# Optimization experiments

Hardware: AMD Instinct MI355X
Metric: run time of the kernel (lower is better)

The kernel has to match this reference:

```python
import jax, jax.numpy as jnp
import numpy as np

D_MODEL = 1024
NHEAD = 16
HEAD_DIM = D_MODEL // NHEAD
B, L = 4, 4096
LN_EPS = 1e-5


def setup_inputs() -> dict:
    key = jax.random.key(0)
    ks = jax.random.split(key, 8)
    x = jax.random.normal(ks[0], (B, L, D_MODEL), dtype=jnp.float32)
    sin = jnp.zeros((L, HEAD_DIM), dtype=jnp.float32)
    cos = jnp.zeros((L, HEAD_DIM), dtype=jnp.float32)
    # decay[:,1,0] is read as per-head lambda in (0,1)
    decay = jax.random.uniform(ks[1], (NHEAD, 2, 1), dtype=jnp.float32)
    scale = 0.02
    Wq = jax.random.normal(ks[2], (D_MODEL, D_MODEL), dtype=jnp.float32) * scale
    Wv = jax.random.normal(ks[3], (D_MODEL, D_MODEL), dtype=jnp.float32) * scale
    Wo = jax.random.normal(ks[4], (D_MODEL, D_MODEL), dtype=jnp.float32) * scale
    Wg = jax.random.normal(ks[5], (D_MODEL, D_MODEL), dtype=jnp.float32) * scale
    ln_g = jnp.ones((D_MODEL,), dtype=jnp.float32)
    ln_b = jnp.zeros((D_MODEL,), dtype=jnp.float32)
    return {"x": x, "sin": sin, "cos": cos, "decay": decay,
            "Wq": Wq, "Wv": Wv, "Wo": Wo, "Wg": Wg,
            "ln_g": ln_g, "ln_b": ln_b}


def _retention(v, lam):
    # v: [B,L,H,Dh], lam: [H] -> cumulative decayed sum over L
    def step(state, v_t):  # state,[B,H,Dh]
        state = lam[None, :, None] * state + v_t
        return state, state
    v_l_first = jnp.swapaxes(v, 0, 1)  # [L,B,H,Dh]
    init = jnp.zeros(v_l_first.shape[1:], dtype=v.dtype)
    _, states = jax.lax.scan(step, init, v_l_first)
    return jnp.swapaxes(states, 0, 1)  # [B,L,H,Dh]


def reference(x, sin, cos, decay, Wq, Wv, Wo, Wg, ln_g, ln_b):
    del sin, cos  # discarded by the module
    Bx, Lx, D = x.shape
    H = decay.shape[0]
    Dh = D // H
    q = (x @ Wq.T).reshape(Bx, Lx, H, Dh)
    v = (x @ Wv.T).reshape(Bx, Lx, H, Dh)
    lam = decay[:, 1, 0]  # [H]
    state = _retention(v, lam)  # [B,L,H,Dh]
    y = (q * state).reshape(Bx, Lx, D)
    # LayerNorm over last dim
    mu = jnp.mean(y, axis=-1, keepdims=True)
    var = jnp.mean(jnp.square(y - mu), axis=-1, keepdims=True)
    y = (y - mu) * jax.lax.rsqrt(var + LN_EPS) * ln_g + ln_b
    gate = jax.nn.silu(x @ Wg.T)
    y = y * gate
    return y @ Wo.T
```

## Files before the change

### kernel.cpp

```cpp
#include <hip/hip_runtime.h>

#define DM    1024
#define LSEQ  4096
#define BATCH 4
#define MROWS (BATCH * LSEQ)
#define MD    ((size_t)MROWS * DM)
#define DD    ((size_t)DM * DM)
#define CHUNK 32
#define NCH   (LSEQ / CHUNK)
#define NCHAIN (BATCH * DM)

typedef __attribute__((ext_vector_type(4))) float  f32x4;
typedef __attribute__((ext_vector_type(8))) __bf16 bf16x8;
typedef __attribute__((ext_vector_type(4))) __bf16 bf16x4;

__device__ __forceinline__ void gload_lds16(const void* g, void* l) {
  __builtin_amdgcn_global_load_lds(
      (const __attribute__((address_space(1))) void*)g,
      (__attribute__((address_space(3))) void*)l, 16, 0, 0);
}

__global__ __launch_bounds__(256) void cvt_bf16(const float* __restrict__ in,
                                                __bf16* __restrict__ out) {
  size_t i = ((size_t)blockIdx.x * 256 + threadIdx.x) * 4;
  f32x4 f = *(const f32x4*)(in + i);
  bf16x4 o;
#pragma unroll
  for (int j = 0; j < 4; ++j) o[j] = (__bf16)f[j];
  *(bf16x4*)(out + i) = o;
}

__global__ __launch_bounds__(256) void cvt_w(const float* __restrict__ s0,
                                             const float* __restrict__ s1,
                                             const float* __restrict__ s2,
                                             const float* __restrict__ s3,
                                             __bf16* __restrict__ dst) {
  const float* sp = (blockIdx.z == 0) ? s0 : (blockIdx.z == 1) ? s1
                  : (blockIdx.z == 2) ? s2 : s3;
  size_t i = ((size_t)blockIdx.x * 256 + threadIdx.x) * 4;
  f32x4 f = *(const f32x4*)(sp + i);
  bf16x4 o;
#pragma unroll
  for (int j = 0; j < 4; ++j) o[j] = (__bf16)f[j];
  *(bf16x4*)(dst + (size_t)blockIdx.z * DD + i) = o;
}


__device__ __forceinline__ int swz(int b) { return b ^ ((b >> 3) & 0x70); }

__device__ __forceinline__ bf16x8 ldf(const char* tile, int row, int k) {
  int lin = (row << 7) + (k << 1);
  return *(const bf16x8*)(tile + swz(lin));
}

__device__ __forceinline__ void stageA_half(const __bf16* Abase, char* tileA,
                                            int h, int k0, int t) {
#pragma unroll
  for (int is = 0; is < 2; ++is) {
    int d = h * 16384 + is * 8192 + t * 16;
    int l = swz(d);
    int lds_r = l >> 7, cb = l & 127;
    int g = ((lds_r >> 6) & 1) * 128 + h * 64 + (lds_r & 63);
    gload_lds16((const char*)Abase + (size_t)g * (DM * 2) + k0 * 2 + cb, tileA + d);
  }
}
__device__ __forceinline__ void stageB_half(const __bf16* Bbase, char* tileB,
                                            int h, int k0, int t) {
#pragma unroll
  for (int is = 0; is < 2; ++is) {
    int d = h * 16384 + is * 8192 + t * 16;
    int l = swz(d);
    int lds_r = l >> 7, cb = l & 127;
    int g = ((lds_r >> 5) & 3) * 64 + h * 32 + (lds_r & 31);
    gload_lds16((const char*)Bbase + (size_t)g * (DM * 2) + k0 * 2 + cb, tileB + d);
  }
}

template <typename OutT>
__global__ __launch_bounds__(512, 2) void gemm_nt(const __bf16* __restrict__ A,
                                                  const __bf16* __restrict__ Wb,
                                                  OutT* __restrict__ Cb) {
  constexpr int K = DM, N = DM, NT = K / 64;
  __shared__ __attribute__((aligned(128))) char lds[131072];

  const __bf16* Wp = Wb + (size_t)blockIdx.z * DD;
  OutT* Cp = Cb + (size_t)blockIdx.z * MD;

  const int orig = blockIdx.y * 4 + blockIdx.x;
  const int sid = (orig & 7) * 32 + (orig >> 3);
  const int bx = sid & 3, by = sid >> 2;
  const int m0 = by * 256, n0 = bx * 256;

  const int t = threadIdx.x, lane = t & 63, wv = t >> 6;
  const int wr = wv >> 2, wc = wv & 3;
  const int lrow = lane & 15, lk8 = (lane >> 4) * 8;

  const __bf16* Abase = A + (size_t)m0 * K;
  const __bf16* Bbase = Wp + (size_t)n0 * K;

  f32x4 acc[8][4] = {};
  bf16x8 a[4][2];
  bf16x8 bq[2][2][2];

  char* buf0 = lds;
  char* buf1 = lds + 65536;

  stageA_half(Abase, buf0,         0, 0, t);
  stageB_half(Bbase, buf0 + 32768, 0, 0, t);
  stageB_half(Bbase, buf0 + 32768, 1, 0, t);
  stageA_half(Abase, buf0,         1, 0, t);
  stageA_half(Abase, buf1,         0, 64, t);
  stageB_half(Bbase, buf1 + 32768, 0, 64, t);
  stageB_half(Bbase, buf1 + 32768, 1, 64, t);
  stageA_half(Abase, buf1,         1, 64, t);
  asm volatile("s_waitcnt vmcnt(12)\n\ts_barrier" ::: "memory");

#define LDA_(mh)                                                        \
  _Pragma("unroll") for (int mf = 0; mf < 4; ++mf)                      \
  _Pragma("unroll") for (int ks = 0; ks < 2; ++ks)                      \
    a[mf][ks] = ldf(At, (mh) * 128 + wr * 64 + mf * 16 + lrow, ks * 32 + lk8);
#define LDB_(nh)                                                        \
  _Pragma("unroll") for (int nf = 0; nf < 2; ++nf)                      \
  _Pragma("unroll") for (int ks = 0; ks < 2; ++ks)                      \
    bq[nh][nf][ks] = ldf(Bt, (nh) * 128 + wc * 32 + nf * 16 + lrow, ks * 32 + lk8);
#define MFMA16_(mh, nh)                                                 \
  __builtin_amdgcn_s_setprio(1);                                        \
  _Pragma("unroll") for (int mf = 0; mf < 4; ++mf)                      \
  _Pragma("unroll") for (int nf = 0; nf < 2; ++nf)                      \
  _Pragma("unroll") for (int ks = 0; ks < 2; ++ks)                      \
    acc[(mh) * 4 + mf][(nh) * 2 + nf] = __builtin_amdgcn_mfma_f32_16x16x32_bf16( \
        a[mf][ks], bq[nh][nf][ks], acc[(mh) * 4 + mf][(nh) * 2 + nf], 0, 0, 0); \
  __builtin_amdgcn_s_setprio(0);
#define VMBAR_(n)                                                       \
  asm volatile("s_waitcnt vmcnt(" #n ")\n\ts_barrier" ::: "memory");
#define BAR_                                                            \
  asm volatile("s_barrier" ::: "memory");

#pragma unroll 1
  for (int kt = 0; kt < NT; ++kt) {
    char* bufc = lds + (kt & 1) * 65536;
    const char* At = bufc;
    const char* Bt = bufc + 32768;
    const int k2 = (kt + 2) << 6;
    const bool s2 = (kt + 2 < NT);

    LDA_(0); LDB_(0);
    MFMA16_(0, 0);
    if (kt < NT - 1) { VMBAR_(10); } else { VMBAR_(2); }

    if (s2) {
      stageA_half(Abase, bufc,         0, k2, t);
      stageB_half(Bbase, bufc + 32768, 0, k2, t);
    }
    LDB_(1);
    MFMA16_(0, 1);
    if (s2) { VMBAR_(12); } else if (kt == NT - 2) { VMBAR_(8); } else { VMBAR_(0); }

    if (s2) stageB_half(Bbase, bufc + 32768, 1, k2, t);
    LDA_(1);
    MFMA16_(1, 0);
    BAR_;

    if (s2) stageA_half(Abase, bufc, 1, k2, t);
    MFMA16_(1, 1);
    if (s2) { VMBAR_(12); } else if (kt == NT - 2) { VMBAR_(4); } else { VMBAR_(0); }
  }
#undef LDA_
#undef LDB_
#undef MFMA16_
#undef VMBAR_
#undef BAR_

#pragma unroll
  for (int mi = 0; mi < 8; ++mi) {
    int r0 = m0 + wr * 128 + (mi >> 2) * 64 + (mi & 3) * 16 + (lane >> 4) * 4;
#pragma unroll
    for (int ni = 0; ni < 4; ++ni) {
      int c0 = n0 + wc * 64 + (ni >> 1) * 32 + (ni & 1) * 16 + (lane & 15);
#pragma unroll
      for (int j = 0; j < 4; ++j) {
        float v = acc[mi][ni][j];
        if constexpr (__is_same(OutT, float))
          Cp[(size_t)(r0 + j) * N + c0] = v;
        else
          Cp[(size_t)(r0 + j) * N + c0] = (__bf16)v;
      }
    }
  }
}

__global__ __launch_bounds__(256) void scan_sum(const __bf16* __restrict__ v,
                                                float* __restrict__ csum,
                                                const float* __restrict__ decay) {
  int tid = blockIdx.x * 256 + threadIdx.x;
  int dg = tid & 255;
  int b  = (tid >> 8) & 3;
  int c  = tid >> 10;
  int d0 = dg * 4;
  float lam = decay[((d0 >> 6) << 1) + 1];
  f32x4 s = {0.f, 0.f, 0.f, 0.f};
  size_t base = ((size_t)b * LSEQ + (size_t)c * CHUNK) * DM + d0;
  for (int t = 0; t < CHUNK; ++t) {
    bf16x4 vv = *(const bf16x4*)(v + base);
    f32x4 vf = {(float)vv[0], (float)vv[1], (float)vv[2], (float)vv[3]};
    s = lam * s + vf;
    base += DM;
  }
  *(f32x4*)(csum + (size_t)c * NCHAIN + b * DM + d0) = s;
}

__global__ __launch_bounds__(256) void scan2(const float* __restrict__ csum,
                                             float* __restrict__ carry,
                                             const float* __restrict__ decay) {
  int i = blockIdx.x * 256 + threadIdx.x;
  int ch0 = i * 4;
  int d0 = ch0 & (DM - 1);
  float lam = decay[((d0 >> 6) << 1) + 1];
  float l2 = lam * lam, l4 = l2 * l2, l8 = l4 * l4, l16 = l8 * l8;
  float lamC = l16 * l16;
  f32x4 cs = {0.f, 0.f, 0.f, 0.f};
  for (int c = 0; c < NCH; ++c) {
    *(f32x4*)(carry + (size_t)c * NCHAIN + ch0) = cs;
    f32x4 sm = *(const f32x4*)(csum + (size_t)c * NCHAIN + ch0);
    cs = lamC * cs + sm;
  }
}

__global__ __launch_bounds__(256) void fuse_chunk(
    const __bf16* __restrict__ qb, const __bf16* __restrict__ vb,
    const __bf16* __restrict__ gb, const float* __restrict__ carry,
    const float* __restrict__ decay, const float* __restrict__ ln_g,
    const float* __restrict__ ln_b, __bf16* __restrict__ y2) {
  const int blk = blockIdx.x;
  const int b = blk >> 7, c = blk & 127;
  const int t = threadIdx.x, lane = t & 63, wv = t >> 6;
  const int d0 = t * 4;
  const float lam = decay[((d0 >> 6) << 1) + 1];
  f32x4 s = *(const f32x4*)(carry + (size_t)c * NCHAIN + b * DM + d0);
  const size_t base0 = ((size_t)b * LSEQ + (size_t)c * CHUNK) * DM + d0;

  __shared__ float sbs[2][32][4];
  __shared__ float stats[32][2];

  f32x4 y[32];
#pragma unroll
  for (int r = 0; r < 32; ++r) {
    size_t base = base0 + (size_t)r * DM;
    bf16x4 v4 = *(const bf16x4*)(vb + base);
    bf16x4 q4 = *(const bf16x4*)(qb + base);
    f32x4 vf = {(float)v4[0], (float)v4[1], (float)v4[2], (float)v4[3]};
    s = lam * s + vf;
    f32x4 yy;
    float su = 0.f, sq = 0.f;
#pragma unroll
    for (int i = 0; i < 4; ++i) {
      float val = (float)q4[i] * s[i];
      yy[i] = val; su += val; sq += val * val;
    }
    y[r] = yy;
#pragma unroll
    for (int o = 32; o > 0; o >>= 1) {
      su += __shfl_xor(su, o);
      sq += __shfl_xor(sq, o);
    }
    if (lane == 0) { sbs[0][r][wv] = su; sbs[1][r][wv] = sq; }
  }
  __syncthreads();
  if (t < 32) {
    float su = sbs[0][t][0] + sbs[0][t][1] + sbs[0][t][2] + sbs[0][t][3];
    float sq = sbs[1][t][0] + sbs[1][t][1] + sbs[1][t][2] + sbs[1][t][3];
    float mu = su * (1.0f / DM);
    float var = sq * (1.0f / DM) - mu * mu;
    stats[t][0] = mu;
    stats[t][1] = rsqrtf(fmaxf(var, 0.0f) + 1e-5f);
  }
  __syncthreads();

  f32x4 lg = *(const f32x4*)(ln_g + d0);
  f32x4 lb = *(const f32x4*)(ln_b + d0);
#pragma unroll
  for (int r = 0; r < 32; ++r) {
    size_t base = base0 + (size_t)r * DM;
    bf16x4 g4 = *(const bf16x4*)(gb + base);
    const float mu = stats[r][0], rstd = stats[r][1];
    bf16x4 o4;
#pragma unroll
    for (int i = 0; i < 4; ++i) {
      float gv = (float)g4[i];
      float gate = gv / (1.0f + __expf(-gv));
      o4[i] = (__bf16)(fmaf((y[r][i] - mu) * rstd, lg[i], lb[i]) * gate);
    }
    *(bf16x4*)(y2 + base) = o4;
  }
}

extern "C" void kernel_launch(void* const* d_in, const int* in_sizes, int n_in,
                              void* d_out, int out_size, void* d_ws, size_t ws_size,
                              hipStream_t stream) {
  const float* x     = (const float*)d_in[0];
  const float* decay = (const float*)d_in[3];
  const float* Wq    = (const float*)d_in[4];
  const float* Wv    = (const float*)d_in[5];
  const float* Wo    = (const float*)d_in[6];
  const float* Wg    = (const float*)d_in[7];
  const float* lng   = (const float*)d_in[8];
  const float* lnb   = (const float*)d_in[9];
  float* out = (float*)d_out;

  char* ws = (char*)d_ws;
  size_t off = 0;
  auto alloc = [&](size_t bytes) -> void* {
    void* p = ws + off;
    off += (bytes + 255) & ~(size_t)255;
    return p;
  };
  __bf16* xb   = (__bf16*)alloc(MD * 2);
  __bf16* w4   = (__bf16*)alloc(4 * DD * 2);
  __bf16* qvg  = (__bf16*)alloc(3 * MD * 2);
  __bf16* y2b  = (__bf16*)alloc(MD * 2);
  float*  csum = (float*)alloc((size_t)NCH * NCHAIN * 4);
  float*  cry  = (float*)alloc((size_t)NCH * NCHAIN * 4);

  cvt_bf16<<<(int)(MD / 1024), 256, 0, stream>>>(x, xb);
  cvt_w<<<dim3((unsigned)(DD / 1024), 1, 4), 256, 0, stream>>>(Wq, Wv, Wg, Wo, w4);

  gemm_nt<__bf16><<<dim3(4, MROWS / 256, 3), 512, 0, stream>>>(xb, w4, qvg);

  scan_sum<<<(BATCH * NCH * (DM / 4)) / 256, 256, 0, stream>>>(qvg + MD, csum, decay);
  scan2<<<(NCHAIN / 4) / 256, 256, 0, stream>>>(csum, cry, decay);

  fuse_chunk<<<BATCH * NCH, 256, 0, stream>>>(qvg, qvg + MD, qvg + 2 * MD, cry,
                                              decay, lng, lnb, y2b);

  gemm_nt<float><<<dim3(4, MROWS / 256, 1), 512, 0, stream>>>(y2b, w4 + 3 * DD, out);
}
```

Measured before the change: 215.4 us.

## Replace tuned 256x256 swizzled GEMM with simple 128x128 double-buffered GEMM

Replaces the hand-scheduled 256x256-tile, 512-thread GEMM with a simpler 128x128-tile, 256-thread kernel. It uses K-step 32, unswizzled LDS tiles and a plain double buffer with a full vmcnt/lgkmcnt wait and barrier each iteration. The aim is higher occupancy (4 blocks per CU) and simpler code. In exchange it loses the LDS swizzle, so bank conflicts become likely, and it gets less data reuse per tile, more barriers, and weaker overlap of loads with MFMA work.

```diff
diff --git a/kernel.cpp b/kernel.cpp
--- a/kernel.cpp
+++ b/kernel.cpp
@@ -46,140 +46,79 @@
 }
 
 
-__device__ __forceinline__ int swz(int b) { return b ^ ((b >> 3) & 0x70); }
-
-__device__ __forceinline__ bf16x8 ldf(const char* tile, int row, int k) {
-  int lin = (row << 7) + (k << 1);
-  return *(const bf16x8*)(tile + swz(lin));
-}
-
-__device__ __forceinline__ void stageA_half(const __bf16* Abase, char* tileA,
-                                            int h, int k0, int t) {
+__device__ __forceinline__ void stage_tile(const __bf16* __restrict__ base,
+                                           __bf16* lds, int k0, int t) {
 #pragma unroll
   for (int is = 0; is < 2; ++is) {
-    int d = h * 16384 + is * 8192 + t * 16;
-    int l = swz(d);
-    int lds_r = l >> 7, cb = l & 127;
-    int g = ((lds_r >> 6) & 1) * 128 + h * 64 + (lds_r & 63);
-    gload_lds16((const char*)Abase + (size_t)g * (DM * 2) + k0 * 2 + cb, tileA + d);
-  }
-}
-__device__ __forceinline__ void stageB_half(const __bf16* Bbase, char* tileB,
-                                            int h, int k0, int t) {
-#pragma unroll
-  for (int is = 0; is < 2; ++is) {
-    int d = h * 16384 + is * 8192 + t * 16;
-    int l = swz(d);
-    int lds_r = l >> 7, cb = l & 127;
-    int g = ((lds_r >> 5) & 3) * 64 + h * 32 + (lds_r & 31);
-    gload_lds16((const char*)Bbase + (size_t)g * (DM * 2) + k0 * 2 + cb, tileB + d);
+    int e = is * 2048 + t * 8;
+    int r = e >> 5, c = e & 31;
+    gload_lds16(base + (size_t)r * DM + k0 + c, lds + e);
   }
 }
 
 template <typename OutT>
-__global__ __launch_bounds__(512, 2) void gemm_nt(const __bf16* __restrict__ A,
+__global__ __launch_bounds__(256, 4) void gemm_nt(const __bf16* __restrict__ A,
                                                   const __bf16* __restrict__ Wb,
                                                   OutT* __restrict__ Cb) {
-  constexpr int K = DM, N = DM, NT = K / 64;
-  __shared__ __attribute__((aligned(128))) char lds[131072];
+  constexpr int K = DM, N = DM, NT = K / 32;
+  __shared__ __bf16 As[2][128 * 32];
+  __shared__ __bf16 Bs[2][128 * 32];
 
   const __bf16* Wp = Wb + (size_t)blockIdx.z * DD;
   OutT* Cp = Cb + (size_t)blockIdx.z * MD;
 
-  const int orig = blockIdx.y * 4 + blockIdx.x;
-  const int sid = (orig & 7) * 32 + (orig >> 3);
-  const int bx = sid & 3, by = sid >> 2;
-  const int m0 = by * 256, n0 = bx * 256;
+  const int orig = blockIdx.y * 8 + blockIdx.x;
+  const int sid = (orig & 7) * 128 + (orig >> 3);
+  const int bx = sid & 7, by = sid >> 3;
+  const int m0 = by * 128, n0 = bx * 128;
 
   const int t = threadIdx.x, lane = t & 63, wv = t >> 6;
-  const int wr = wv >> 2, wc = wv & 3;
-  const int lrow = lane & 15, lk8 = (lane >> 4) * 8;
+  const int wr = wv >> 1, wc = wv & 1;
+  const int lrow = lane & 15, koff = (lane >> 4) * 8;
 
   const __bf16* Abase = A + (size_t)m0 * K;
   const __bf16* Bbase = Wp + (size_t)n0 * K;
 
-  f32x4 acc[8][4] = {};
-  bf16x8 a[4][2];
-  bf16x8 bq[2][2][2];
-
-  char* buf0 = lds;
-  char* buf1 = lds + 65536;
-
-  stageA_half(Abase, buf0,         0, 0, t);
-  stageB_half(Bbase, buf0 + 32768, 0, 0, t);
-  stageB_half(Bbase, buf0 + 32768, 1, 0, t);
-  stageA_half(Abase, buf0,         1, 0, t);
-  stageA_half(Abase, buf1,         0, 64, t);
-  stageB_half(Bbase, buf1 + 32768, 0, 64, t);
-  stageB_half(Bbase, buf1 + 32768, 1, 64, t);
-  stageA_half(Abase, buf1,         1, 64, t);
-  asm volatile("s_waitcnt vmcnt(12)\n\ts_barrier" ::: "memory");
-
-#define LDA_(mh)                                                        \
-  _Pragma("unroll") for (int mf = 0; mf < 4; ++mf)                      \
-  _Pragma("unroll") for (int ks = 0; ks < 2; ++ks)                      \
-    a[mf][ks] = ldf(At, (mh) * 128 + wr * 64 + mf * 16 + lrow, ks * 32 + lk8);
-#define LDB_(nh)                                                        \
-  _Pragma("unroll") for (int nf = 0; nf < 2; ++nf)                      \
-  _Pragma("unroll") for (int ks = 0; ks < 2; ++ks)                      \
-    bq[nh][nf][ks] = ldf(Bt, (nh) * 128 + wc * 32 + nf * 16 + lrow, ks * 32 + lk8);
-#define MFMA16_(mh, nh)                                                 \
-  __builtin_amdgcn_s_setprio(1);                                        \
-  _Pragma("unroll") for (int mf = 0; mf < 4; ++mf)                      \
-  _Pragma("unroll") for (int nf = 0; nf < 2; ++nf)                      \
-  _Pragma("unroll") for (int ks = 0; ks < 2; ++ks)                      \
-    acc[(mh) * 4 + mf][(nh) * 2 + nf] = __builtin_amdgcn_mfma_f32_16x16x32_bf16( \
-        a[mf][ks], bq[nh][nf][ks], acc[(mh) * 4 + mf][(nh) * 2 + nf], 0, 0, 0); \
-  __builtin_amdgcn_s_setprio(0);
-#define VMBAR_(n)                                                       \
-  asm volatile("s_waitcnt vmcnt(" #n ")\n\ts_barrier" ::: "memory");
-#define BAR_                                                            \
-  asm volatile("s_barrier" ::: "memory");
+  f32x4 acc[4][4] = {};
+  bf16x8 a[4], b[4];
+
+  stage_tile(Abase, As[0], 0, t);
+  stage_tile(Bbase, Bs[0], 0, t);
+  asm volatile("s_waitcnt vmcnt(0)\n\ts_barrier" ::: "memory");
 
 #pragma unroll 1
   for (int kt = 0; kt < NT; ++kt) {
-    char* bufc = lds + (kt & 1) * 65536;
-    const char* At = bufc;
-    const char* Bt = bufc + 32768;
-    const int k2 = (kt + 2) << 6;
-    const bool s2 = (kt + 2 < NT);
-
-    LDA_(0); LDB_(0);
-    MFMA16_(0, 0);
-    if (kt < NT - 1) { VMBAR_(10); } else { VMBAR_(2); }
-
-    if (s2) {
-      stageA_half(Abase, bufc,         0, k2, t);
-      stageB_half(Bbase, bufc + 32768, 0, k2, t);
-    }
-    LDB_(1);
-    MFMA16_(0, 1);
-    if (s2) { VMBAR_(12); } else if (kt == NT - 2) { VMBAR_(8); } else { VMBAR_(0); }
-
-    if (s2) stageB_half(Bbase, bufc + 32768, 1, k2, t);
-    LDA_(1);
-    MFMA16_(1, 0);
-    BAR_;
-
-    if (s2) stageA_half(Abase, bufc, 1, k2, t);
-    MFMA16_(1, 1);
-    if (s2) { VMBAR_(12); } else if (kt == NT - 2) { VMBAR_(4); } else { VMBAR_(0); }
-  }
-#undef LDA_
-#undef LDB_
-#undef MFMA16_
-#undef VMBAR_
-#undef BAR_
-
-#pragma unroll
-  for (int mi = 0; mi < 8; ++mi) {
-    int r0 = m0 + wr * 128 + (mi >> 2) * 64 + (mi & 3) * 16 + (lane >> 4) * 4;
-#pragma unroll
-    for (int ni = 0; ni < 4; ++ni) {
-      int c0 = n0 + wc * 64 + (ni >> 1) * 32 + (ni & 1) * 16 + (lane & 15);
+    const int cur = kt & 1, nxt = cur ^ 1;
+    if (kt + 1 < NT) {
+      stage_tile(Abase, As[nxt], (kt + 1) * 32, t);
+      stage_tile(Bbase, Bs[nxt], (kt + 1) * 32, t);
+    }
+#pragma unroll
+    for (int mf = 0; mf < 4; ++mf)
+      a[mf] = *(const bf16x8*)&As[cur][(wr * 64 + mf * 16 + lrow) * 32 + koff];
+#pragma unroll
+    for (int nf = 0; nf < 4; ++nf)
+      b[nf] = *(const bf16x8*)&Bs[cur][(wc * 64 + nf * 16 + lrow) * 32 + koff];
+    __builtin_amdgcn_s_setprio(1);
+#pragma unroll
+    for (int mf = 0; mf < 4; ++mf)
+#pragma unroll
+      for (int nf = 0; nf < 4; ++nf)
+        acc[mf][nf] = __builtin_amdgcn_mfma_f32_16x16x32_bf16(
+            a[mf], b[nf], acc[mf][nf], 0, 0, 0);
+    __builtin_amdgcn_s_setprio(0);
+    asm volatile("s_waitcnt vmcnt(0) lgkmcnt(0)\n\ts_barrier" ::: "memory");
+  }
+
+#pragma unroll
+  for (int mf = 0; mf < 4; ++mf) {
+    int r0 = m0 + wr * 64 + mf * 16 + (lane >> 4) * 4;
+#pragma unroll
+    for (int nf = 0; nf < 4; ++nf) {
+      int c0 = n0 + wc * 64 + nf * 16 + (lane & 15);
 #pragma unroll
       for (int j = 0; j < 4; ++j) {
-        float v = acc[mi][ni][j];
+        float v = acc[mf][nf][j];
         if constexpr (__is_same(OutT, float))
           Cp[(size_t)(r0 + j) * N + c0] = v;
         else
@@ -324,7 +263,7 @@
   cvt_bf16<<<(int)(MD / 1024), 256, 0, stream>>>(x, xb);
   cvt_w<<<dim3((unsigned)(DD / 1024), 1, 4), 256, 0, stream>>>(Wq, Wv, Wg, Wo, w4);
 
-  gemm_nt<__bf16><<<dim3(4, MROWS / 256, 3), 512, 0, stream>>>(xb, w4, qvg);
+  gemm_nt<__bf16><<<dim3(8, MROWS / 128, 3), 256, 0, stream>>>(xb, w4, qvg);
 
   scan_sum<<<(BATCH * NCH * (DM / 4)) / 256, 256, 0, stream>>>(qvg + MD, csum, decay);
   scan2<<<(NCHAIN / 4) / 256, 256, 0, stream>>>(csum, cry, decay);
@@ -332,5 +271,5 @@
   fuse_chunk<<<BATCH * NCH, 256, 0, stream>>>(qvg, qvg + MD, qvg + 2 * MD, cry,
                                               decay, lng, lnb, y2b);
 
-  gemm_nt<float><<<dim3(4, MROWS / 256, 1), 512, 0, stream>>>(y2b, w4 + 3 * DD, out);
-}
+  gemm_nt<float><<<dim3(8, MROWS / 128, 1), 256, 0, stream>>>(y2b, w4 + 3 * DD, out);
+}
```

Result: slower. 237.4 us (+10.2%).

## Restructure GEMM main loop with single-tile LDS prefetch and register double-buffering

Applied to the files above, without the earlier changes.

Replaces the half-tile, two-steps-ahead LDS staging with whole-tile staging one step ahead. It adds ping-pong register fragments, so LDS reads for the next half overlap the MFMAs of the current half. Explicit lgkmcnt waits and sched_barriers pin the instruction order, and launch bounds drop to one block per CU to relax register limits. The aim is to hide LDS-read latency behind matrix math. The cost is a full vmcnt(0) barrier every iteration and a shorter global-load lookahead.

```diff
diff --git a/kernel.cpp b/kernel.cpp
--- a/kernel.cpp
+++ b/kernel.cpp
@@ -53,31 +53,19 @@
   return *(const bf16x8*)(tile + swz(lin));
 }
 
-__device__ __forceinline__ void stageA_half(const __bf16* Abase, char* tileA,
-                                            int h, int k0, int t) {
-#pragma unroll
-  for (int is = 0; is < 2; ++is) {
-    int d = h * 16384 + is * 8192 + t * 16;
+__device__ __forceinline__ void stage_tile(const __bf16* __restrict__ base,
+                                           char* tile, int k0, int t) {
+#pragma unroll
+  for (int is = 0; is < 4; ++is) {
+    int d = is * 8192 + t * 16;
     int l = swz(d);
-    int lds_r = l >> 7, cb = l & 127;
-    int g = ((lds_r >> 6) & 1) * 128 + h * 64 + (lds_r & 63);
-    gload_lds16((const char*)Abase + (size_t)g * (DM * 2) + k0 * 2 + cb, tileA + d);
-  }
-}
-__device__ __forceinline__ void stageB_half(const __bf16* Bbase, char* tileB,
-                                            int h, int k0, int t) {
-#pragma unroll
-  for (int is = 0; is < 2; ++is) {
-    int d = h * 16384 + is * 8192 + t * 16;
-    int l = swz(d);
-    int lds_r = l >> 7, cb = l & 127;
-    int g = ((lds_r >> 5) & 3) * 64 + h * 32 + (lds_r & 31);
-    gload_lds16((const char*)Bbase + (size_t)g * (DM * 2) + k0 * 2 + cb, tileB + d);
+    int row = l >> 7, cb = l & 127;
+    gload_lds16((const char*)base + (size_t)row * (DM * 2) + k0 * 2 + cb, tile + d);
   }
 }
 
 template <typename OutT>
-__global__ __launch_bounds__(512, 2) void gemm_nt(const __bf16* __restrict__ A,
+__global__ __launch_bounds__(512, 1) void gemm_nt(const __bf16* __restrict__ A,
                                                   const __bf16* __restrict__ Wb,
                                                   OutT* __restrict__ Cb) {
   constexpr int K = DM, N = DM, NT = K / 64;
@@ -99,77 +87,68 @@
   const __bf16* Bbase = Wp + (size_t)n0 * K;
 
   f32x4 acc[8][4] = {};
-  bf16x8 a[4][2];
-  bf16x8 bq[2][2][2];
-
-  char* buf0 = lds;
-  char* buf1 = lds + 65536;
-
-  stageA_half(Abase, buf0,         0, 0, t);
-  stageB_half(Bbase, buf0 + 32768, 0, 0, t);
-  stageB_half(Bbase, buf0 + 32768, 1, 0, t);
-  stageA_half(Abase, buf0,         1, 0, t);
-  stageA_half(Abase, buf1,         0, 64, t);
-  stageB_half(Bbase, buf1 + 32768, 0, 64, t);
-  stageB_half(Bbase, buf1 + 32768, 1, 64, t);
-  stageA_half(Abase, buf1,         1, 64, t);
-  asm volatile("s_waitcnt vmcnt(12)\n\ts_barrier" ::: "memory");
-
-#define LDA_(mh)                                                        \
+  bf16x8 a0[4][2], a1[4][2];
+  bf16x8 b0[2][2], b1[2][2];
+
+#define LDA_(dst, mh, tile)                                             \
   _Pragma("unroll") for (int mf = 0; mf < 4; ++mf)                      \
   _Pragma("unroll") for (int ks = 0; ks < 2; ++ks)                      \
-    a[mf][ks] = ldf(At, (mh) * 128 + wr * 64 + mf * 16 + lrow, ks * 32 + lk8);
-#define LDB_(nh)                                                        \
+    dst[mf][ks] = ldf(tile, wr * 128 + (mh) * 64 + mf * 16 + lrow, ks * 32 + lk8);
+#define LDB_(dst, nh, tile)                                             \
   _Pragma("unroll") for (int nf = 0; nf < 2; ++nf)                      \
   _Pragma("unroll") for (int ks = 0; ks < 2; ++ks)                      \
-    bq[nh][nf][ks] = ldf(Bt, (nh) * 128 + wc * 32 + nf * 16 + lrow, ks * 32 + lk8);
-#define MFMA16_(mh, nh)                                                 \
+    dst[nf][ks] = ldf(tile, wc * 64 + (nh) * 32 + nf * 16 + lrow, ks * 32 + lk8);
+#define MFMA16_(av, bv, mh, nh)                                         \
   __builtin_amdgcn_s_setprio(1);                                        \
   _Pragma("unroll") for (int mf = 0; mf < 4; ++mf)                      \
   _Pragma("unroll") for (int nf = 0; nf < 2; ++nf)                      \
   _Pragma("unroll") for (int ks = 0; ks < 2; ++ks)                      \
     acc[(mh) * 4 + mf][(nh) * 2 + nf] = __builtin_amdgcn_mfma_f32_16x16x32_bf16( \
-        a[mf][ks], bq[nh][nf][ks], acc[(mh) * 4 + mf][(nh) * 2 + nf], 0, 0, 0); \
+        av[mf][ks], bv[nf][ks], acc[(mh) * 4 + mf][(nh) * 2 + nf], 0, 0, 0); \
   __builtin_amdgcn_s_setprio(0);
-#define VMBAR_(n)                                                       \
-  asm volatile("s_waitcnt vmcnt(" #n ")\n\ts_barrier" ::: "memory");
-#define BAR_                                                            \
-  asm volatile("s_barrier" ::: "memory");
+#define SB_ __builtin_amdgcn_sched_barrier(0);
+#define LGKM_(n)                                                        \
+  asm volatile("s_waitcnt lgkmcnt(" #n ")" ::: "memory"); SB_
+
+  stage_tile(Abase, lds,         0, t);
+  stage_tile(Bbase, lds + 32768, 0, t);
+  asm volatile("s_waitcnt vmcnt(0)\n\ts_barrier" ::: "memory");
+  SB_
+  LDB_(b0, 0, lds + 32768); SB_
+  LDA_(a0, 0, lds); SB_
 
 #pragma unroll 1
   for (int kt = 0; kt < NT; ++kt) {
     char* bufc = lds + (kt & 1) * 65536;
-    const char* At = bufc;
-    const char* Bt = bufc + 32768;
-    const int k2 = (kt + 2) << 6;
-    const bool s2 = (kt + 2 < NT);
-
-    LDA_(0); LDB_(0);
-    MFMA16_(0, 0);
-    if (kt < NT - 1) { VMBAR_(10); } else { VMBAR_(2); }
-
-    if (s2) {
-      stageA_half(Abase, bufc,         0, k2, t);
-      stageB_half(Bbase, bufc + 32768, 0, k2, t);
-    }
-    LDB_(1);
-    MFMA16_(0, 1);
-    if (s2) { VMBAR_(12); } else if (kt == NT - 2) { VMBAR_(8); } else { VMBAR_(0); }
-
-    if (s2) stageB_half(Bbase, bufc + 32768, 1, k2, t);
-    LDA_(1);
-    MFMA16_(1, 0);
-    BAR_;
-
-    if (s2) stageA_half(Abase, bufc, 1, k2, t);
-    MFMA16_(1, 1);
-    if (s2) { VMBAR_(12); } else if (kt == NT - 2) { VMBAR_(4); } else { VMBAR_(0); }
+    char* bufn = lds + ((kt & 1) ^ 1) * 65536;
+    const bool s1 = (kt + 1 < NT);
+
+    if (s1) {
+      stage_tile(Abase, bufn,         (kt + 1) * 64, t);
+      stage_tile(Bbase, bufn + 32768, (kt + 1) * 64, t);
+    }
+    SB_
+    LDB_(b1, 1, bufc + 32768); SB_
+    LDA_(a1, 1, bufc); SB_
+
+    LGKM_(12)
+    MFMA16_(a0, b0, 0, 0); SB_
+    LGKM_(8)
+    MFMA16_(a0, b1, 0, 1); SB_
+    LGKM_(0)
+    asm volatile("s_waitcnt vmcnt(0)\n\ts_barrier" ::: "memory");
+    SB_
+
+    if (s1) { LDA_(a0, 0, bufn); SB_ }
+    MFMA16_(a1, b0, 1, 0); SB_
+    if (s1) { LDB_(b0, 0, bufn + 32768); SB_ }
+    MFMA16_(a1, b1, 1, 1); SB_
   }
 #undef LDA_
 #undef LDB_
 #undef MFMA16_
-#undef VMBAR_
-#undef BAR_
+#undef LGKM_
+#undef SB_
 
 #pragma unroll
   for (int mi = 0; mi < 8; ++mi) {
```

Measured after the change: 249.1 us. 15.6% more time.
